# Performance work log

Hardware: AMD Instinct MI355X
Metric: run time of the kernel (lower is better)

The kernel has to match this reference:

```python
import jax, jax.numpy as jnp
import numpy as np

B, S, E = 2, 4096, 1024
H = 16
W = 256  # attention_window == chunk size; attn width = 3*W


def _chunk3(x):
    # x: [b, nc, w, h, d] -> stack (prev, cur, next) chunks on last axis: [b, nc, w, h, d, 3]
    prev = jnp.pad(x[:, :-1], ((0, 0), (1, 0), (0, 0), (0, 0), (0, 0)))
    nxt = jnp.pad(x[:, 1:], ((0, 0), (0, 1), (0, 0), (0, 0), (0, 0)))
    return jnp.stack([prev, x, nxt], axis=-1)


def setup_inputs() -> dict:
    key = jax.random.key(0)
    ks = jax.random.split(key, 4)
    hs = jax.random.normal(ks[0], (B, S, E), jnp.float32)

    def lin(k):
        kw, kb = jax.random.split(k)
        return (jax.random.normal(kw, (E, E), jnp.float32) * 0.02,
                jax.random.normal(kb, (E,), jnp.float32) * 0.02)

    Wq, bq = lin(ks[1])
    Wk, bk = lin(ks[2])
    Wv, bv = lin(ks[3])
    return {"hidden_states": hs, "Wq": Wq, "bq": bq, "Wk": Wk, "bk": bk, "Wv": Wv, "bv": bv}


def reference(hidden_states, Wq, bq, Wk, bk, Wv, bv):
    b, s, e = hidden_states.shape
    h, w = H, W
    d = e // h
    nc = s // w  # number of non-overlapping chunks

    # torch nn.Linear: y = x @ W.T + b ; q scaled by 1/sqrt(head_dim)
    q = (hidden_states @ Wq.T + bq) * (1.0 / np.sqrt(d))
    k = hidden_states @ Wk.T + bk
    v = hidden_states @ Wv.T + bv
    q = q.reshape(b, s, h, d)
    k = k.reshape(b, s, h, d)
    v = v.reshape(b, s, h, d)

    # ---- sliding_chunks_no_overlap_matmul_qk ----
    cq = q.reshape(b, nc, w, h, d)
    ck3 = _chunk3(k.reshape(b, nc, w, h, d))  # [b,nc,w,h,d,3]
    # [b,nc,w,h,3,w] -> [b,s,h,3w]
    scores = jnp.einsum('bcxhd,bcyhde->bcxhey', cq, ck3).reshape(b, s, h, 3 * w)

    # ---- mask_invalid_locations (same math as Longformer's helper) ----
    ii = jnp.arange(w)[:, None]
    cc = jnp.arange(w + 1)[None, :]
    beg_mask = cc < (w - ii)   # [w, w+1] applied to first w rows, first w+1 cols
    end_mask = cc >= (w - ii)  # flipped mask, last w rows, last w+1 cols
    neg_inf = jnp.array(-jnp.inf, scores.dtype)
    beg = jnp.where(beg_mask[None, :, None, :], neg_inf, scores[:, :w, :, :w + 1])
    scores = scores.at[:, :w, :, :w + 1].set(beg)
    end = jnp.where(end_mask[None, :, None, :], neg_inf, scores[:, s - w:, :, 3 * w - (w + 1):])
    scores = scores.at[:, s - w:, :, 3 * w - (w + 1):].set(end)

    # softmax in float32 (as in original), cast back
    probs = jax.nn.softmax(scores.astype(jnp.float32), axis=-1).astype(hidden_states.dtype)

    # ---- sliding_chunks_no_overlap_matmul_pv ----
    cp = probs.reshape(b, nc, w, h, 3, w)          # bcwhpd (d = key pos in chunk)
    cv3 = _chunk3(v.reshape(b, nc, w, h, d))       # bcdhep (d = pos, e = head_dim, p = 3)
    attn = jnp.einsum('bcwhpd,bcdhep->bcwhe', cp, cv3).reshape(b, s, h, d)

    return attn.reshape(b, s, e)
```

## Files before the change

### kernel.cpp

```cpp
#include <hip/hip_runtime.h>
#include <math.h>

#define BB  2
#define SS  4096
#define EE  1024
#define HH  16
#define DD  64
#define WW  256
#define NCC 16
#define MTOT (BB*SS)

typedef __attribute__((ext_vector_type(4))) float f32x4;
typedef __attribute__((ext_vector_type(8))) short bf16x8;

__device__ __forceinline__ void gl_lds16(const void* g, void* l) {
  __builtin_amdgcn_global_load_lds(
      (const __attribute__((address_space(1))) unsigned int*)g,
      (__attribute__((address_space(3))) unsigned int*)l,
      16, 0, 0);
}

__device__ __forceinline__ unsigned bf16rne(float f) {
  unsigned u = __float_as_uint(f);
  return (u + (((u >> 16) & 1u) + 0x7fffu)) >> 16;
}

__device__ __forceinline__ unsigned long long pack64(unsigned a, unsigned b,
                                                     unsigned c2, unsigned d) {
  return (unsigned long long)(a | (b << 16)) |
         ((unsigned long long)(c2 | (d << 16)) << 32);
}

__global__ __launch_bounds__(256) void split_all(
    const float* __restrict__ hs, const float* __restrict__ Wq,
    const float* __restrict__ Wk, const float* __restrict__ Wv,
    unsigned short* __restrict__ Ahi, unsigned short* __restrict__ Alo,
    unsigned short* __restrict__ Wqh, unsigned short* __restrict__ Wql,
    unsigned short* __restrict__ Wkh, unsigned short* __restrict__ Wkl,
    unsigned short* __restrict__ Wvh, unsigned short* __restrict__ Wvl)
{
  const int bx = blockIdx.x;
  const float* src; unsigned short *hi, *lo; size_t blk;
  if (bx < 8192)       { src = hs; hi = Ahi; lo = Alo; blk = bx; }
  else if (bx < 9216)  { src = Wq; hi = Wqh; lo = Wql; blk = bx - 8192; }
  else if (bx < 10240) { src = Wk; hi = Wkh; lo = Wkl; blk = bx - 9216; }
  else                 { src = Wv; hi = Wvh; lo = Wvl; blk = bx - 10240; }

  const size_t i = blk * 256 + threadIdx.x;
  const float4 v = ((const float4*)src)[i];
  float f[4] = {v.x, v.y, v.z, v.w};
  unsigned short h[4], l[4];
  #pragma unroll
  for (int j = 0; j < 4; ++j) {
    unsigned u  = __float_as_uint(f[j]);
    unsigned uh = u & 0xFFFF0000u;
    h[j] = (unsigned short)(uh >> 16);
    float r = f[j] - __uint_as_float(uh);
    unsigned ur = __float_as_uint(r);
    ur += ((ur >> 16) & 1u) + 0x7FFFu;
    l[j] = (unsigned short)(ur >> 16);
  }
  *(ushort4*)&hi[4*i] = make_ushort4(h[0], h[1], h[2], h[3]);
  *(ushort4*)&lo[4*i] = make_ushort4(l[0], l[1], l[2], l[3]);
}

struct ProjArgs {
  const unsigned short* Wh;
  const unsigned short* Wl;
  const float* bias;
  unsigned short* outHi;
  unsigned short* outLo;
  float scale;
};

__global__ __launch_bounds__(512) void mfma_proj(
    const unsigned short* __restrict__ Ahi,
    const unsigned short* __restrict__ Alo,
    ProjArgs p0, ProjArgs p1, ProjArgs p2)
{
  __shared__ __align__(16) union {
    unsigned short stage[2][24576];
    unsigned short ep[128][136];
  } sh;

  const int tid  = threadIdx.x;
  const int lane = tid & 63;
  const int wid  = tid >> 6;
  const int wr   = wid >> 1;
  const int wc   = wid & 1;
  const int m0   = blockIdx.x * 256, n0 = blockIdx.y * 128;
  const ProjArgs P = (blockIdx.z == 0) ? p0 : ((blockIdx.z == 1) ? p1 : p2);

  const int qA0 = tid, qA1 = 512 + tid;
  const int rowA0 = ((qA0 >> 5) << 3) | (qA0 & 7), kcA0 = (qA0 >> 3) & 3;
  const int rowA1 = ((qA1 >> 5) << 3) | (qA1 & 7), kcA1 = (qA1 >> 3) & 3;
  const int rowB  = rowA0, kcB = kcA0;

  const size_t aoff0 = (size_t)(m0 + rowA0) * 2048 + (size_t)(kcA0 * 16);
  const size_t aoff1 = (size_t)(m0 + rowA1) * 2048 + (size_t)(kcA1 * 16);
  const size_t boff  = (size_t)(n0 + rowB)  * 2048 + (size_t)(kcB  * 16);

  const int dstA0 = wid * 1024;
  const int dstA1 = 8192 + wid * 1024;
  const int dstB  = wid * 1024;

  const char* gAh = (const char*)Ahi;
  const char* gAl = (const char*)Alo;
  const char* gBh = (const char*)P.Wh;
  const char* gBl = (const char*)P.Wl;

  const int fr = lane & 15;
  const int kc = lane >> 4;
  int a_o[4], b_o[4];
  #pragma unroll
  for (int f = 0; f < 4; ++f) {
    int r = wr * 64 + f * 16 + fr;
    a_o[f] = ((r >> 3) << 9) | (kc << 7) | ((r & 7) << 4);
    r = wc * 64 + f * 16 + fr;
    b_o[f] = ((r >> 3) << 9) | (kc << 7) | ((r & 7) << 4);
  }

  f32x4 acc[4][4];
  #pragma unroll
  for (int i = 0; i < 4; ++i)
    #pragma unroll
    for (int j = 0; j < 4; ++j) acc[i][j] = (f32x4){0.f, 0.f, 0.f, 0.f};

  char* const Lp = (char*)&sh.stage[0][0];
  #define PL(b, p) (Lp + ((b) * 49152 + (p)))

  #define STAGE(buf, ks) { const size_t kb = (size_t)(ks) * 64; \
    gl_lds16(gAh + aoff0 + kb, PL(buf,0)     + dstA0); \
    gl_lds16(gAh + aoff1 + kb, PL(buf,0)     + dstA1); \
    gl_lds16(gAl + aoff0 + kb, PL(buf,16384) + dstA0); \
    gl_lds16(gAl + aoff1 + kb, PL(buf,16384) + dstA1); \
    gl_lds16(gBh + boff  + kb, PL(buf,32768) + dstB); \
    gl_lds16(gBl + boff  + kb, PL(buf,40960) + dstB); }

  #define COMPUTE(buf) { \
    bf16x8 ah[4], bh[4]; \
    _Pragma("unroll") \
    for (int f = 0; f < 4; ++f) { \
      ah[f] = *(const bf16x8*)(PL(buf,0)     + a_o[f]); \
      bh[f] = *(const bf16x8*)(PL(buf,32768) + b_o[f]); \
    } \
    asm volatile("s_waitcnt lgkmcnt(0)" ::: "memory"); \
    __builtin_amdgcn_sched_barrier(0); \
    bf16x8 al[4], bl[4]; \
    _Pragma("unroll") \
    for (int f = 0; f < 4; ++f) { \
      al[f] = *(const bf16x8*)(PL(buf,16384) + a_o[f]); \
      bl[f] = *(const bf16x8*)(PL(buf,40960) + b_o[f]); \
    } \
    __builtin_amdgcn_s_setprio(1); \
    _Pragma("unroll") \
    for (int i = 0; i < 4; ++i) \
      _Pragma("unroll") \
      for (int j = 0; j < 4; ++j) \
        acc[i][j] = __builtin_amdgcn_mfma_f32_16x16x32_bf16(ah[i], bh[j], acc[i][j], 0,0,0); \
    __builtin_amdgcn_s_setprio(0); \
    asm volatile("s_waitcnt lgkmcnt(0)" ::: "memory"); \
    __builtin_amdgcn_sched_barrier(0); \
    __builtin_amdgcn_s_setprio(1); \
    _Pragma("unroll") \
    for (int i = 0; i < 4; ++i) \
      _Pragma("unroll") \
      for (int j = 0; j < 4; ++j) \
        acc[i][j] = __builtin_amdgcn_mfma_f32_16x16x32_bf16(ah[i], bl[j], acc[i][j], 0,0,0); \
    _Pragma("unroll") \
    for (int i = 0; i < 4; ++i) \
      _Pragma("unroll") \
      for (int j = 0; j < 4; ++j) \
        acc[i][j] = __builtin_amdgcn_mfma_f32_16x16x32_bf16(al[i], bh[j], acc[i][j], 0,0,0); \
    __builtin_amdgcn_s_setprio(0); }

  STAGE(0, 0);
  STAGE(1, 1);
  #pragma unroll 2
  for (int ks = 0; ks < 31; ++ks) {
    const int b = ks & 1;
    asm volatile("s_waitcnt vmcnt(6)" ::: "memory");
    __builtin_amdgcn_sched_barrier(0);
    __builtin_amdgcn_s_barrier();
    COMPUTE(b);
    __builtin_amdgcn_s_barrier();
    if (ks + 2 < 32) STAGE(b, ks + 2);
  }
  asm volatile("s_waitcnt vmcnt(0)" ::: "memory");
  __builtin_amdgcn_sched_barrier(0);
  __builtin_amdgcn_s_barrier();
  COMPUTE(1);
  #undef PL
  #undef STAGE
  #undef COMPUTE

  const int r4 = (lane >> 4) << 2;
  #pragma unroll
  for (int hh = 0; hh < 2; ++hh) {
    #pragma unroll
    for (int plane = 0; plane < 2; ++plane) {
      __syncthreads();
      if ((wr >> 1) == hh) {
        #pragma unroll
        for (int j = 0; j < 4; ++j) {
          const int col_l = wc*64 + j*16 + fr;
          const float bv = P.bias[n0 + col_l];
          #pragma unroll
          for (int i = 0; i < 4; ++i) {
            const int rl0 = (wr & 1)*64 + i*16 + r4;
            #pragma unroll
            for (int v = 0; v < 4; ++v) {
              const float val = (acc[i][j][v] + bv) * P.scale;
              const unsigned u = __float_as_uint(val);
              unsigned sv;
              if (plane == 0) { sv = u >> 16; }
              else {
                const float rres = val - __uint_as_float(u & 0xFFFF0000u);
                unsigned ur = __float_as_uint(rres);
                ur += ((ur >> 16) & 1u) + 0x7FFFu; sv = ur >> 16;
              }
              const int rl = rl0 + v;
              sh.ep[rl][(((col_l >> 3) ^ (rl & 7)) << 3) + (col_l & 7)] =
                  (unsigned short)sv;
            }
          }
        }
      }
      __syncthreads();
      unsigned short* const OUT = plane ? P.outLo : P.outHi;
      #pragma unroll
      for (int u2 = 0; u2 < 4; ++u2) {
        const int chunk = u2 * 512 + tid;
        const int rr = chunk >> 4, c16 = chunk & 15;
        const bf16x8 vv = *(const bf16x8*)&sh.ep[rr][(c16 ^ (rr & 7)) << 3];
        *(bf16x8*)&OUT[(size_t)(m0 + hh*128 + rr) * EE + n0 + c16*8] = vv;
      }
    }
  }
}

__global__ __launch_bounds__(256, 2) void attn_mfma(
    const unsigned short* __restrict__ Qh_g, const unsigned short* __restrict__ Ql_g,
    const unsigned short* __restrict__ Kh_g, const unsigned short* __restrict__ Kl_g,
    const unsigned short* __restrict__ Vh_g, const unsigned short* __restrict__ Vl_g,
    float* __restrict__ Og)
{
  __shared__ __align__(16) unsigned short Kf[2][2048];
  __shared__ __align__(16) unsigned short Vt[2][2048];
  __shared__ unsigned long long Pscr[4][256];

  const int c = blockIdx.x, h = blockIdx.y, b = blockIdx.z;
  const int tid = threadIdx.x;
  const int lane = tid & 63, wid = tid >> 6;
  const int g = lane >> 4, lq = lane & 15;

  const size_t qrow0 = (size_t)(b * NCC + c) * WW;
  const int colh = h * DD;

  bf16x8 qfh[4][2], qfl[4][2];
  #pragma unroll
  for (int s = 0; s < 4; ++s)
    #pragma unroll
    for (int ch = 0; ch < 2; ++ch) {
      const size_t off = (qrow0 + wid*64 + s*16 + lq) * EE + colh + ch*32 + g*8;
      qfh[s][ch] = *(const bf16x8*)(Qh_g + off);
      qfl[s][ch] = *(const bf16x8*)(Ql_g + off);
    }

  f32x4 Oa[4][4];
  #pragma unroll
  for (int i = 0; i < 4; ++i)
    #pragma unroll
    for (int j = 0; j < 4; ++j) Oa[i][j] = (f32x4){0.f, 0.f, 0.f, 0.f};
  float m[4], lsum[4];
  #pragma unroll
  for (int s = 0; s < 4; ++s) { m[s] = -1e30f; lsum[s] = 0.f; }

  const int kK = 16*(wid & 1) + lq;
  const int dK = 32*(wid >> 1) + g*8;
  const int stv = tid >> 5, idxv = tid & 31;
  const int kV = 16*(stv >> 2) + (idxv >> 1);
  const int dV = 16*(stv & 3) + 8*(idxv & 1);
  const int C0  = ((dV >> 4) << 6) | ((kV >> 3) << 4) | (dV & 15);
  const int swW = (((dV >> 4) & 1) << 2) | (((kV >> 3) & 1) << 1) | ((dV >> 3) & 1);
  const int vel = kV & 7;

  const long krow0_base = (long)qrow0 - WW;
  const int t0 = (c == 0) ? 8 : 0;
  const int tN = (c == NCC-1) ? 16 : 24;

  uint4 rkh, rkl, rvh, rvl;
  {
    const long kr = krow0_base + (long)t0*32;
    const size_t offK = (size_t)(kr + kK) * EE + colh + dK;
    const size_t offV = (size_t)(kr + kV) * EE + colh + dV;
    rkh = *(const uint4*)(Kh_g + offK); rkl = *(const uint4*)(Kl_g + offK);
    rvh = *(const uint4*)(Vh_g + offV); rvl = *(const uint4*)(Vl_g + offV);
  }

  for (int tt = t0; tt < tN; ++tt) {
    __syncthreads();
    *(uint4*)&Kf[0][wid*512 + lane*8] = rkh;
    *(uint4*)&Kf[1][wid*512 + lane*8] = rkl;
    {
      const unsigned hw[4] = {rvh.x, rvh.y, rvh.z, rvh.w};
      const unsigned lw[4] = {rvl.x, rvl.y, rvl.z, rvl.w};
      #pragma unroll
      for (int t = 0; t < 8; ++t) {
        const int ii = C0*8 + ((t ^ swW) << 3) + vel;
        Vt[0][ii] = (unsigned short)(hw[t >> 1] >> ((t & 1) * 16));
        Vt[1][ii] = (unsigned short)(lw[t >> 1] >> ((t & 1) * 16));
      }
    }
    __syncthreads();

    if (tt + 1 < tN) {
      const long kr = krow0_base + (long)(tt+1)*32;
      const size_t offK = (size_t)(kr + kK) * EE + colh + dK;
      const size_t offV = (size_t)(kr + kV) * EE + colh + dV;
      rkh = *(const uint4*)(Kh_g + offK); rkl = *(const uint4*)(Kl_g + offK);
      rvh = *(const uint4*)(Vh_g + offV); rvl = *(const uint4*)(Vl_g + offV);
    }

    bf16x8 kfh[2][2], kfl[2][2];
    #pragma unroll
    for (int f = 0; f < 4; ++f) {
      const int o = f*512 + lane*8;
      kfh[f & 1][f >> 1] = *(const bf16x8*)&Kf[0][o];
      kfl[f & 1][f >> 1] = *(const bf16x8*)&Kf[1][o];
    }

    bf16x8 vfh[4], vfl[4];
    #pragma unroll
    for (int ds = 0; ds < 4; ++ds) {
      const int rch = ds*64 + g*16 + lq;
      const int rsw = (((rch >> 6) & 1) << 2) | (((rch >> 4) & 1) << 1) | ((rch >> 3) & 1);
      vfh[ds] = *(const bf16x8*)&Vt[0][(rch ^ rsw) * 8];
      vfl[ds] = *(const bf16x8*)&Vt[1][(rch ^ rsw) * 8];
    }

    #pragma unroll
    for (int s = 0; s < 4; ++s) {
      f32x4 ac0 = (f32x4){0.f,0.f,0.f,0.f}, ac1 = (f32x4){0.f,0.f,0.f,0.f};
      #pragma unroll
      for (int ch = 0; ch < 2; ++ch) {
        ac0 = __builtin_amdgcn_mfma_f32_16x16x32_bf16(kfh[0][ch], qfh[s][ch], ac0, 0,0,0);
        ac0 = __builtin_amdgcn_mfma_f32_16x16x32_bf16(kfh[0][ch], qfl[s][ch], ac0, 0,0,0);
        ac0 = __builtin_amdgcn_mfma_f32_16x16x32_bf16(kfl[0][ch], qfh[s][ch], ac0, 0,0,0);
        ac1 = __builtin_amdgcn_mfma_f32_16x16x32_bf16(kfh[1][ch], qfh[s][ch], ac1, 0,0,0);
        ac1 = __builtin_amdgcn_mfma_f32_16x16x32_bf16(kfh[1][ch], qfl[s][ch], ac1, 0,0,0);
        ac1 = __builtin_amdgcn_mfma_f32_16x16x32_bf16(kfl[1][ch], qfh[s][ch], ac1, 0,0,0);
      }

      float tmax = fmaxf(fmaxf(fmaxf(ac0[0],ac0[1]), fmaxf(ac0[2],ac0[3])),
                         fmaxf(fmaxf(ac1[0],ac1[1]), fmaxf(ac1[2],ac1[3])));
      tmax = fmaxf(tmax, __shfl_xor(tmax, 16));
      tmax = fmaxf(tmax, __shfl_xor(tmax, 32));
      const float mo = m[s];
      const float mn = fmaxf(mo, tmax);
      m[s] = mn;
      const float sc = __expf(mo - mn);
      float pv[8];
      #pragma unroll
      for (int r = 0; r < 4; ++r) { pv[r] = __expf(ac0[r] - mn); pv[4+r] = __expf(ac1[r] - mn); }
      float ps = 0.f;
      #pragma unroll
      for (int r = 0; r < 8; ++r) ps += pv[r];
      lsum[s] = lsum[s] * sc + ps;
      #pragma unroll
      for (int ds = 0; ds < 4; ++ds) Oa[ds][s] *= sc;

      unsigned hb[8], lb[8];
      #pragma unroll
      for (int r = 0; r < 8; ++r) {
        hb[r] = bf16rne(pv[r]);
        const float rr = pv[r] - __uint_as_float(hb[r] << 16);
        lb[r] = bf16rne(rr);
      }
      const int pq = (g >> 1)*32 + lq*2 + (g & 1);
      Pscr[wid][pq]            = pack64(hb[0],hb[1],hb[2],hb[3]);
      Pscr[wid][pq + 64]       = pack64(hb[4],hb[5],hb[6],hb[7]);
      Pscr[wid][128 + pq]      = pack64(lb[0],lb[1],lb[2],lb[3]);
      Pscr[wid][128 + pq + 64] = pack64(lb[4],lb[5],lb[6],lb[7]);
      asm volatile("" ::: "memory");
      union U8 { unsigned long long q[2]; bf16x8 v; };
      U8 uh, ul;
      uh.q[0] = Pscr[wid][lane*2];       uh.q[1] = Pscr[wid][lane*2 + 1];
      ul.q[0] = Pscr[wid][128 + lane*2]; ul.q[1] = Pscr[wid][128 + lane*2 + 1];
      const bf16x8 pbh = uh.v;
      const bf16x8 pbl = ul.v;

      #pragma unroll
      for (int ds = 0; ds < 4; ++ds) {
        Oa[ds][s] = __builtin_amdgcn_mfma_f32_16x16x32_bf16(vfh[ds], pbh, Oa[ds][s], 0,0,0);
        Oa[ds][s] = __builtin_amdgcn_mfma_f32_16x16x32_bf16(vfl[ds], pbh, Oa[ds][s], 0,0,0);
        Oa[ds][s] = __builtin_amdgcn_mfma_f32_16x16x32_bf16(vfh[ds], pbl, Oa[ds][s], 0,0,0);
      }
    }
  }

  #pragma unroll
  for (int s = 0; s < 4; ++s) {
    float ls = lsum[s];
    ls += __shfl_xor(ls, 16);
    ls += __shfl_xor(ls, 32);
    const int x = wid*64 + s*16 + lq;
    const float nz = (c == 0) ? (float)x
                   : ((c == NCC-1) ? (float)(WW - 1 - x) : 0.f);
    ls += nz * __expf(0.f - m[s]);
    const float inv = 1.f / ls;
    float* op = Og + (qrow0 + x) * EE + colh;
    #pragma unroll
    for (int ds = 0; ds < 4; ++ds) {
      float4 r;
      r.x = Oa[ds][s][0]*inv; r.y = Oa[ds][s][1]*inv;
      r.z = Oa[ds][s][2]*inv; r.w = Oa[ds][s][3]*inv;
      *(float4*)(op + ds*16 + g*4) = r;
    }
  }
}

extern "C" void kernel_launch(void* const* d_in, const int* in_sizes, int n_in,
                              void* d_out, int out_size, void* d_ws, size_t ws_size,
                              hipStream_t stream) {
    const float* hs = (const float*)d_in[0];
    const float* Wq = (const float*)d_in[1];
    const float* bq = (const float*)d_in[2];
    const float* Wk = (const float*)d_in[3];
    const float* bk = (const float*)d_in[4];
    const float* Wv = (const float*)d_in[5];
    const float* bv = (const float*)d_in[6];
    float* out = (float*)d_out;

    const size_t mat  = (size_t)MTOT * EE;
    const size_t wmat = (size_t)EE * EE;

    unsigned short* w = (unsigned short*)d_ws;
    unsigned short* Ahi = w;            unsigned short* Alo = Ahi + mat;
    unsigned short* Wqh = Alo + mat;    unsigned short* Wql = Wqh + wmat;
    unsigned short* Wkh = Wql + wmat;   unsigned short* Wkl = Wkh + wmat;
    unsigned short* Wvh = Wkl + wmat;   unsigned short* Wvl = Wvh + wmat;
    unsigned short* Qhb = Wvl + wmat;   unsigned short* Qlb = Qhb + mat;
    unsigned short* Khb = Qlb + mat;    unsigned short* Klb = Khb + mat;
    unsigned short* Vhb = Klb + mat;    unsigned short* Vlb = Vhb + mat;

    split_all<<<8192 + 3*1024, 256, 0, stream>>>(
        hs, Wq, Wk, Wv, Ahi, Alo, Wqh, Wql, Wkh, Wkl, Wvh, Wvl);

    ProjArgs pq{Wqh, Wql, bq, Qhb, Qlb, 0.125f};
    ProjArgs pk{Wkh, Wkl, bk, Khb, Klb, 1.0f};
    ProjArgs pv{Wvh, Wvl, bv, Vhb, Vlb, 1.0f};
    dim3 g(MTOT/256, EE/128, 3);
    mfma_proj<<<g, 512, 0, stream>>>(Ahi, Alo, pq, pk, pv);

    dim3 ga(NCC, HH, BB);
    attn_mfma<<<ga, 256, 0, stream>>>(Qhb, Qlb, Khb, Klb, Vhb, Vlb, out);
}
```

Baseline: 316.3 us.

## Triple-buffer projection GEMM LDS staging and prefetch next fragments across iterations

Changes the projection GEMM main loop from double to triple LDS buffering, so global loads run two k-steps ahead. The loop is unrolled by six with ping-pong register fragments, so the high-part A/B fragments for the next step are read from LDS while the current step's MFMAs execute. The LDS waits and barriers are rearranged to match. This raises LDS use to 144KB, which may lower occupancy, and adds register pressure from the extra fragment set.

```diff
diff --git a/kernel.cpp b/kernel.cpp
--- a/kernel.cpp
+++ b/kernel.cpp
@@ -79,7 +79,7 @@
     ProjArgs p0, ProjArgs p1, ProjArgs p2)
 {
   __shared__ __align__(16) union {
-    unsigned short stage[2][24576];
+    unsigned short stage[3][24576];
     unsigned short ep[128][136];
   } sh;
 
@@ -137,62 +137,83 @@
     gl_lds16(gBh + boff  + kb, PL(buf,32768) + dstB); \
     gl_lds16(gBl + boff  + kb, PL(buf,40960) + dstB); }
 
-  #define COMPUTE(buf) { \
-    bf16x8 ah[4], bh[4]; \
+  bf16x8 ah0[4], bh0[4], ah1[4], bh1[4];
+  bf16x8 al[4], bl[4];
+
+  #define RD_C1(AH, BH, buf) { \
     _Pragma("unroll") \
     for (int f = 0; f < 4; ++f) { \
-      ah[f] = *(const bf16x8*)(PL(buf,0)     + a_o[f]); \
-      bh[f] = *(const bf16x8*)(PL(buf,32768) + b_o[f]); \
-    } \
-    asm volatile("s_waitcnt lgkmcnt(0)" ::: "memory"); \
-    __builtin_amdgcn_sched_barrier(0); \
-    bf16x8 al[4], bl[4]; \
+      AH[f] = *(const bf16x8*)(PL(buf,0)     + a_o[f]); \
+      BH[f] = *(const bf16x8*)(PL(buf,32768) + b_o[f]); \
+    } }
+  #define RD_C2(buf) { \
     _Pragma("unroll") \
     for (int f = 0; f < 4; ++f) { \
       al[f] = *(const bf16x8*)(PL(buf,16384) + a_o[f]); \
       bl[f] = *(const bf16x8*)(PL(buf,40960) + b_o[f]); \
-    } \
-    __builtin_amdgcn_s_setprio(1); \
+    } }
+
+  #define MM16(AA, BBV) { \
     _Pragma("unroll") \
     for (int i = 0; i < 4; ++i) \
       _Pragma("unroll") \
       for (int j = 0; j < 4; ++j) \
-        acc[i][j] = __builtin_amdgcn_mfma_f32_16x16x32_bf16(ah[i], bh[j], acc[i][j], 0,0,0); \
-    __builtin_amdgcn_s_setprio(0); \
-    asm volatile("s_waitcnt lgkmcnt(0)" ::: "memory"); \
+        acc[i][j] = __builtin_amdgcn_mfma_f32_16x16x32_bf16(AA[i], BBV[j], acc[i][j], 0,0,0); }
+
+  #define ITER(KS, B, BN, AHc, BHc, AHn, BHn, VM, DOSTAGE, DONEXT) { \
+    RD_C2(B); \
+    __builtin_amdgcn_sched_barrier(0); \
+    asm volatile("s_waitcnt lgkmcnt(8)" ::: "memory");    \
     __builtin_amdgcn_sched_barrier(0); \
     __builtin_amdgcn_s_setprio(1); \
-    _Pragma("unroll") \
-    for (int i = 0; i < 4; ++i) \
-      _Pragma("unroll") \
-      for (int j = 0; j < 4; ++j) \
-        acc[i][j] = __builtin_amdgcn_mfma_f32_16x16x32_bf16(ah[i], bl[j], acc[i][j], 0,0,0); \
-    _Pragma("unroll") \
-    for (int i = 0; i < 4; ++i) \
-      _Pragma("unroll") \
-      for (int j = 0; j < 4; ++j) \
-        acc[i][j] = __builtin_amdgcn_mfma_f32_16x16x32_bf16(al[i], bh[j], acc[i][j], 0,0,0); \
-    __builtin_amdgcn_s_setprio(0); }
+    MM16(AHc, BHc);                                       \
+    __builtin_amdgcn_s_setprio(0); \
+    __builtin_amdgcn_sched_barrier(0); \
+    asm volatile("s_waitcnt lgkmcnt(0)" ::: "memory");    \
+    __builtin_amdgcn_sched_barrier(0); \
+    __builtin_amdgcn_s_barrier();                         \
+    if (DOSTAGE) STAGE(B, (KS)+3); \
+    if (VM == 12)     { asm volatile("s_waitcnt vmcnt(12)" ::: "memory"); } \
+    else if (VM == 6) { asm volatile("s_waitcnt vmcnt(6)"  ::: "memory"); } \
+    else if (VM == 0) { asm volatile("s_waitcnt vmcnt(0)"  ::: "memory"); } \
+    if (VM >= 0) { __builtin_amdgcn_sched_barrier(0); __builtin_amdgcn_s_barrier(); } \
+    if (DONEXT) RD_C1(AHn, BHn, BN); \
+    __builtin_amdgcn_s_setprio(1); \
+    MM16(AHc, bl);                                        \
+    MM16(al, BHc);                                        \
+    __builtin_amdgcn_s_setprio(0); \
+  }
 
   STAGE(0, 0);
   STAGE(1, 1);
-  #pragma unroll 2
-  for (int ks = 0; ks < 31; ++ks) {
-    const int b = ks & 1;
-    asm volatile("s_waitcnt vmcnt(6)" ::: "memory");
-    __builtin_amdgcn_sched_barrier(0);
-    __builtin_amdgcn_s_barrier();
-    COMPUTE(b);
-    __builtin_amdgcn_s_barrier();
-    if (ks + 2 < 32) STAGE(b, ks + 2);
-  }
-  asm volatile("s_waitcnt vmcnt(0)" ::: "memory");
+  STAGE(2, 2);
+  asm volatile("s_waitcnt vmcnt(12)" ::: "memory");
   __builtin_amdgcn_sched_barrier(0);
   __builtin_amdgcn_s_barrier();
-  COMPUTE(1);
+  RD_C1(ah0, bh0, 0);
+
+  for (int kk = 0; kk < 24; kk += 6) {
+    ITER(kk+0, 0, 1, ah0, bh0, ah1, bh1, 12, 1, 1);
+    ITER(kk+1, 1, 2, ah1, bh1, ah0, bh0, 12, 1, 1);
+    ITER(kk+2, 2, 0, ah0, bh0, ah1, bh1, 12, 1, 1);
+    ITER(kk+3, 0, 1, ah1, bh1, ah0, bh0, 12, 1, 1);
+    ITER(kk+4, 1, 2, ah0, bh0, ah1, bh1, 12, 1, 1);
+    ITER(kk+5, 2, 0, ah1, bh1, ah0, bh0, 12, 1, 1);
+  }
+  ITER(24, 0, 1, ah0, bh0, ah1, bh1, 12, 1, 1);
+  ITER(25, 1, 2, ah1, bh1, ah0, bh0, 12, 1, 1);
+  ITER(26, 2, 0, ah0, bh0, ah1, bh1, 12, 1, 1);
+  ITER(27, 0, 1, ah1, bh1, ah0, bh0, 12, 1, 1);
+  ITER(28, 1, 2, ah0, bh0, ah1, bh1, 12, 1, 1);
+  ITER(29, 2, 0, ah1, bh1, ah0, bh0,  6, 0, 1);
+  ITER(30, 0, 1, ah0, bh0, ah1, bh1,  0, 0, 1);
+  ITER(31, 1, 2, ah1, bh1, ah0, bh0, -1, 0, 0);
   #undef PL
   #undef STAGE
-  #undef COMPUTE
+  #undef RD_C1
+  #undef RD_C2
+  #undef MM16
+  #undef ITER
 
   const int r4 = (lane >> 4) << 2;
   #pragma unroll
```

Result: no change. 315.0 us (-0.4%).
